# Kernel tuning notes

Hardware: AMD Instinct MI355X
Metric: run time of the kernel (lower is better)

## Reference

```python
import jax, jax.numpy as jnp
import numpy as np

LN_EPS = 1e-5  # torch.nn.LayerNorm default

QLEN, MLEN, BATCH, D_MODEL = 1024, 1024, 8, 1024


def _ft_matrix(qlen, klen):
    """Real part of the causal Fourier matrix (imag part never contributes:
    the input is real and the module takes .real of the product)."""
    ft_len = klen - qlen + 1
    m = jnp.arange(qlen, dtype=jnp.float32)
    k = jnp.arange(ft_len, dtype=jnp.float32)
    base = jnp.cos((2.0 * float(np.pi)) * jnp.outer(m, k) / float(ft_len))
    base = base / float(np.sqrt(ft_len))                      # [qlen, ft_len]
    mat = jnp.pad(base, ((0, 0), (klen - ft_len, 0)))          # left-pad -> [qlen, klen]
    # row i rolled left by (qlen - 1 - i), vectorized as a gather
    shift = (qlen - 1) - jnp.arange(qlen)                      # [qlen]
    cols = (jnp.arange(klen)[None, :] + shift[:, None]) % klen  # [qlen, klen]
    mat = jnp.take_along_axis(mat, cols, axis=1)
    rows = jnp.arange(qlen)[:, None]
    js = jnp.arange(klen)[None, :]
    # tril(diagonal=klen-qlen) AND triu(0)  (same_length=True)
    mask = (js <= rows + (klen - qlen)) & (js >= rows)
    return jnp.where(mask, mat, jnp.float32(0.0))


def setup_inputs() -> dict:
    key = jax.random.key(0)
    k1, k2, k3 = jax.random.split(key, 3)
    return {
        "dec_inp": jax.random.normal(k1, (QLEN, BATCH, D_MODEL), dtype=jnp.float32),
        "pos_emb": jax.random.normal(k2, (QLEN + MLEN, 1, D_MODEL), dtype=jnp.float32),
        "mems": jax.random.normal(k3, (MLEN, BATCH, D_MODEL), dtype=jnp.float32),
        "gamma": jnp.ones((D_MODEL,), dtype=jnp.float32),
        "beta": jnp.zeros((D_MODEL,), dtype=jnp.float32),
        "add_position": 1,
    }


def reference(dec_inp, pos_emb, mems, gamma, beta, add_position):
    qlen = dec_inp.shape[0]
    klen = qlen + mems.shape[0]
    cat = jnp.concatenate([mems, dec_inp], axis=0)  # [klen, b, d]
    if add_position:
        cat = cat + pos_emb  # dropout is identity in eval mode
    ft_mat = _ft_matrix(qlen, klen)                 # [qlen, klen]
    ft = jnp.einsum('ml,lbd->mbd', ft_mat, cat)     # real part of complex matmul
    x = dec_inp + ft / float(np.sqrt(klen))
    mu = jnp.mean(x, axis=-1, keepdims=True)
    var = jnp.var(x, axis=-1, keepdims=True)
    return gamma * (x - mu) * jax.lax.rsqrt(var + LN_EPS) + beta
```

## Files before the change

### kernel.cpp

```cpp
#include <hip/hip_runtime.h>
#include <hip/hip_bf16.h>

#define QLEN   1024
#define MLEN   1024
#define KLEN   2048
#define BATCH  8
#define DMODEL 1024
#define NCOLS  (BATCH * DMODEL)
#define FTLEN  1025

#define BM 128
#define BN 256
#define BK 64
#define NT 18

typedef __attribute__((ext_vector_type(4))) float f32x4;
typedef __attribute__((ext_vector_type(8))) short bf16x8;

typedef __attribute__((address_space(1))) const unsigned int as1_u32;
typedef __attribute__((address_space(3))) unsigned int as3_u32;

static __device__ __forceinline__ unsigned short f2bf(float f) {
    unsigned int u = __builtin_bit_cast(unsigned int, f);
    return (unsigned short)((u + 0x7fffu + ((u >> 16) & 1u)) >> 16);
}
static __device__ __forceinline__ float bf2f(unsigned short s) {
    return __builtin_bit_cast(float, (unsigned int)s << 16);
}
static __device__ __forceinline__ unsigned int packbf(float lo, float hi) {
    return (unsigned int)f2bf(lo) | ((unsigned int)f2bf(hi) << 16);
}

__global__ __launch_bounds__(256) void prep_fused(
    const float* __restrict__ dec, const float* __restrict__ pos,
    const float* __restrict__ mems, const int* __restrict__ addp,
    unsigned short* __restrict__ catT, unsigned short* __restrict__ W)
{
    const int tid = threadIdx.x;
    if (blockIdx.z == 8) {
        const int bchunk = (blockIdx.y * 32 + blockIdx.x) * 4;
#pragma unroll
        for (int r = 0; r < 4; ++r) {
            const int idx = (bchunk + r) * 256 + tid;
            const int m = idx >> 9;
            const int k4 = (idx & 511) * 4;
            union { unsigned short s[4]; int2 v; } u;
#pragma unroll
            for (int j = 0; j < 4; ++j) {
                const int k = k4 + j;
                const int t = k - m;
                float w = 0.0f;
                if (t >= 0 && t < FTLEN) {
                    const int rr = (m * t) % FTLEN;
                    const float x = (float)rr * (1.0f / (float)FTLEN);
                    float c;
                    asm("v_cos_f32 %0, %1" : "=v"(c) : "v"(x));
                    w = c * 0.03123475237772121f;
                }
                u.s[j] = f2bf(w);
            }
            *reinterpret_cast<int2*>(&W[(size_t)m * KLEN + k4]) = u.v;
        }
        return;
    }

    __shared__ unsigned int T2[32 * 68];
    const int lt = blockIdx.x, dt = blockIdx.y, b = blockIdx.z;
    const int l0 = lt * 64, d0 = dt * 64;
    const int add_position = addp[0];

    const int dloc  = (tid & 15) * 4;
    const int lhalf = tid >> 4;

    float4 vc[2][2];
#pragma unroll
    for (int p = 0; p < 2; ++p)
#pragma unroll
        for (int jl = 0; jl < 2; ++jl) {
            const int l = l0 + p * 32 + lhalf * 2 + jl;
            const float* src = (l < MLEN)
                ? (mems + (size_t)l * NCOLS + b * DMODEL + d0 + dloc)
                : (dec + (size_t)(l - MLEN) * NCOLS + b * DMODEL + d0 + dloc);
            vc[p][jl] = *reinterpret_cast<const float4*>(src);
        }
    if (add_position) {
#pragma unroll
        for (int p = 0; p < 2; ++p)
#pragma unroll
            for (int jl = 0; jl < 2; ++jl) {
                const int l = l0 + p * 32 + lhalf * 2 + jl;
                float4 pv = *reinterpret_cast<const float4*>(
                    pos + (size_t)l * DMODEL + d0 + dloc);
                vc[p][jl].x += pv.x; vc[p][jl].y += pv.y;
                vc[p][jl].z += pv.z; vc[p][jl].w += pv.w;
            }
    }
#pragma unroll
    for (int p = 0; p < 2; ++p) {
        const int lp = p * 16 + lhalf;
        uint4 w;
        w.x = packbf(vc[p][0].x, vc[p][1].x);
        w.y = packbf(vc[p][0].y, vc[p][1].y);
        w.z = packbf(vc[p][0].z, vc[p][1].z);
        w.w = packbf(vc[p][0].w, vc[p][1].w);
        *reinterpret_cast<uint4*>(&T2[lp * 68 + dloc]) = w;
    }
    __syncthreads();
    const int d = tid >> 2;
    const size_t n = (size_t)b * DMODEL + d0 + d;
#pragma unroll
    for (int q = 0; q < 2; ++q) {
        const int c8 = (tid & 3) + 4 * q;
        uint4 o;
        o.x = T2[(c8 * 4 + 0) * 68 + d];
        o.y = T2[(c8 * 4 + 1) * 68 + d];
        o.z = T2[(c8 * 4 + 2) * 68 + d];
        o.w = T2[(c8 * 4 + 3) * 68 + d];
        *reinterpret_cast<uint4*>(&catT[n * KLEN + l0 + c8 * 8]) = o;
    }
}

__global__ __launch_bounds__(512) void gemm_band10(
    const unsigned short* __restrict__ W,
    const unsigned short* __restrict__ catT,
    const float* __restrict__ dec,
    unsigned short* __restrict__ xout)
{
    __shared__ unsigned short Alds[3][BM * BK];
    __shared__ unsigned short Blds[3][BN * BK];

    const int tid = threadIdx.x;
    const int wave = tid >> 6, lane = tid & 63;

    const int bid = blockIdx.x;
    const int xcd = bid & 7;
    const int kk = bid >> 3;
    const int m_idx = kk >> 2;
    const int n_idx = xcd * 4 + (kk & 3);
    const int m0 = m_idx * BM, n0 = n_idx * BN;
    const int wm = wave >> 2, wn = wave & 3;

    f32x4 acc[4][4];
    for (int i = 0; i < 4; ++i)
        for (int j = 0; j < 4; ++j)
            acc[i][j] = (f32x4){0.f, 0.f, 0.f, 0.f};

    const int srow = tid >> 3;
    const int scol = (((tid & 7) ^ ((tid >> 3) & 7)) * 8);
    const int fr = lane & 15;
    const int kg = lane >> 4;
    const int rswz = (fr & 7) * 8;

#define STAGE_LOAD_A(S, T, P) do {                                              \
    const int k0_ = m0 + (T) * BK;                                              \
    const int row = (P) * 64 + srow;                                            \
    __builtin_amdgcn_global_load_lds(                                           \
        (as1_u32*)(const void*)(W + (size_t)(m0 + row) * KLEN + k0_ + scol),    \
        (as3_u32*)(void*)(&Alds[S][row * BK + scol]), 16, 0, 0);                \
} while (0)
#define STAGE_LOAD_B(S, T, P) do {                                              \
    const int k0_ = m0 + (T) * BK;                                              \
    const int row = (P) * 64 + srow;                                            \
    __builtin_amdgcn_global_load_lds(                                           \
        (as1_u32*)(const void*)(catT + (size_t)(n0 + row) * KLEN + k0_ + scol), \
        (as3_u32*)(void*)(&Blds[S][row * BK + scol]), 16, 0, 0);                \
} while (0)
#define STAGE_ALL(S, T) do {                                                    \
    STAGE_LOAD_A(S, T, 0); STAGE_LOAD_A(S, T, 1);                               \
    STAGE_LOAD_B(S, T, 0); STAGE_LOAD_B(S, T, 1);                               \
    STAGE_LOAD_B(S, T, 2); STAGE_LOAD_B(S, T, 3);                               \
} while (0)

    STAGE_ALL(0, 0);
    STAGE_ALL(1, 1);

    for (int t = 0; t < NT; ++t) {
        if (t == NT - 1)
            asm volatile("s_waitcnt vmcnt(0)" ::: "memory");
        else
            asm volatile("s_waitcnt vmcnt(6)" ::: "memory");
        __builtin_amdgcn_s_barrier();

        const unsigned short* Ab = Alds[t % 3];
        const unsigned short* Bb = Blds[t % 3];
        const int s2 = (t + 2) % 3;
        const bool pf = (t + 2 < NT);

        {
            bf16x8 a[4], b[4];
#pragma unroll
            for (int f = 0; f < 4; ++f)
                a[f] = *reinterpret_cast<const bf16x8*>(
                    Ab + (wm * 64 + f * 16 + fr) * BK + ((kg * 8) ^ rswz));
#pragma unroll
            for (int f = 0; f < 4; ++f)
                b[f] = *reinterpret_cast<const bf16x8*>(
                    Bb + (wn * 64 + f * 16 + fr) * BK + ((kg * 8) ^ rswz));
            if (pf) { STAGE_LOAD_A(s2, t + 2, 0); STAGE_LOAD_B(s2, t + 2, 0); STAGE_LOAD_B(s2, t + 2, 1); }
            __builtin_amdgcn_s_setprio(1);
#pragma unroll
            for (int fm = 0; fm < 4; ++fm)
#pragma unroll
                for (int fn = 0; fn < 4; ++fn)
                    acc[fm][fn] = __builtin_amdgcn_mfma_f32_16x16x32_bf16(
                        a[fm], b[fn], acc[fm][fn], 0, 0, 0);
            __builtin_amdgcn_s_setprio(0);
        }
        {
            bf16x8 a[4], b[4];
#pragma unroll
            for (int f = 0; f < 4; ++f)
                a[f] = *reinterpret_cast<const bf16x8*>(
                    Ab + (wm * 64 + f * 16 + fr) * BK + ((32 + kg * 8) ^ rswz));
#pragma unroll
            for (int f = 0; f < 4; ++f)
                b[f] = *reinterpret_cast<const bf16x8*>(
                    Bb + (wn * 64 + f * 16 + fr) * BK + ((32 + kg * 8) ^ rswz));
            if (pf) { STAGE_LOAD_A(s2, t + 2, 1); STAGE_LOAD_B(s2, t + 2, 2); STAGE_LOAD_B(s2, t + 2, 3); }
            __builtin_amdgcn_s_setprio(1);
#pragma unroll
            for (int fm = 0; fm < 4; ++fm)
#pragma unroll
                for (int fn = 0; fn < 4; ++fn)
                    acc[fm][fn] = __builtin_amdgcn_mfma_f32_16x16x32_bf16(
                        a[fm], b[fn], acc[fm][fn], 0, 0, 0);
            __builtin_amdgcn_s_setprio(0);
        }
    }
#undef STAGE_ALL
#undef STAGE_LOAD_A
#undef STAGE_LOAD_B

    const float inv = 0.022097086912079612f;
    const int col16 = lane & 15, rquad = lane >> 4;
#pragma unroll
    for (int fm = 0; fm < 4; ++fm)
#pragma unroll
        for (int fn = 0; fn < 4; ++fn)
#pragma unroll
            for (int j = 0; j < 4; ++j) {
                const int m = m0 + wm * 64 + fm * 16 + rquad * 4 + j;
                const int n = n0 + wn * 64 + fn * 16 + col16;
                const size_t o = (size_t)m * NCOLS + n;
                xout[o] = f2bf(dec[o] + acc[fm][fn][j] * inv);
            }
}

__global__ __launch_bounds__(256) void layernorm_rows(
    const unsigned short* __restrict__ x,
    const float* __restrict__ gamma, const float* __restrict__ beta,
    float* __restrict__ out)
{
    __shared__ float ps[4], pq[4];
    const int row = blockIdx.x;
    const int tid = threadIdx.x;
    const size_t base = (size_t)row * DMODEL + tid * 4;
    ushort4 u = *reinterpret_cast<const ushort4*>(x + base);
    float vx = bf2f(u.x), vy = bf2f(u.y), vz = bf2f(u.z), vw = bf2f(u.w);
    float s  = vx + vy + vz + vw;
    float sq = vx * vx + vy * vy + vz * vz + vw * vw;
    for (int off = 32; off > 0; off >>= 1) {
        s  += __shfl_down(s, off);
        sq += __shfl_down(sq, off);
    }
    const int wave = tid >> 6, lane = tid & 63;
    if (lane == 0) { ps[wave] = s; pq[wave] = sq; }
    __syncthreads();
    if (tid == 0) {
        float ts = ps[0] + ps[1] + ps[2] + ps[3];
        float tq = pq[0] + pq[1] + pq[2] + pq[3];
        float mu = ts * (1.0f / DMODEL);
        float var = tq * (1.0f / DMODEL) - mu * mu;
        ps[0] = mu;
        pq[0] = rsqrtf(var + 1e-5f);
    }
    __syncthreads();
    const float mu = ps[0], rs = pq[0];
    float4 g  = *reinterpret_cast<const float4*>(gamma + tid * 4);
    float4 be = *reinterpret_cast<const float4*>(beta + tid * 4);
    float4 o;
    o.x = g.x * (vx - mu) * rs + be.x;
    o.y = g.y * (vy - mu) * rs + be.y;
    o.z = g.z * (vz - mu) * rs + be.z;
    o.w = g.w * (vw - mu) * rs + be.w;
    *reinterpret_cast<float4*>(out + base) = o;
}

extern "C" void kernel_launch(void* const* d_in, const int* in_sizes, int n_in,
                              void* d_out, int out_size, void* d_ws, size_t ws_size,
                              hipStream_t stream)
{
    const float* dec   = (const float*)d_in[0];
    const float* pos   = (const float*)d_in[1];
    const float* mems  = (const float*)d_in[2];
    const float* gamma = (const float*)d_in[3];
    const float* beta  = (const float*)d_in[4];
    const int*   addp  = (const int*)d_in[5];
    float* out = (float*)d_out;

    unsigned short* catT = (unsigned short*)d_ws;
    unsigned short* Wmat = catT + (size_t)NCOLS * KLEN;
    unsigned short* x    = Wmat + (size_t)QLEN * KLEN;

    prep_fused<<<dim3(32, 16, 9), 256, 0, stream>>>(dec, pos, mems, addp, catT, Wmat);
    gemm_band10<<<256, 512, 0, stream>>>(Wmat, catT, dec, x);
    layernorm_rows<<<8192, 256, 0, stream>>>(x, gamma, beta, out);
}
```

Baseline: 60.48 us.

## Reshape banded GEMM tile to 256x128 with 4 waves of 128x64 each

The GEMM block tile changes from 128x256 with 8 waves to 256x128 with 4 waves, and each wave now computes a 128x64 sub-tile with 32 accumulators. The K-band per block grows to 20 steps because the band width follows BM. The aim is more MFMA work per LDS fragment load and fewer waves to synchronise. The cost is extra K work across the wider band, heavier register pressure, and lower occupancy.

```diff
diff --git a/kernel.cpp b/kernel.cpp
--- a/kernel.cpp
+++ b/kernel.cpp
@@ -9,10 +9,10 @@
 #define NCOLS  (BATCH * DMODEL)
 #define FTLEN  1025
 
-#define BM 128
-#define BN 256
+#define BM 256
+#define BN 128
 #define BK 64
-#define NT 18
+#define NT 20
 
 typedef __attribute__((ext_vector_type(4))) float f32x4;
 typedef __attribute__((ext_vector_type(8))) short bf16x8;
@@ -120,7 +120,7 @@
     }
 }
 
-__global__ __launch_bounds__(512) void gemm_band10(
+__global__ __launch_bounds__(256, 1) void gemm_band11(
     const unsigned short* __restrict__ W,
     const unsigned short* __restrict__ catT,
     const float* __restrict__ dec,
@@ -135,13 +135,15 @@
     const int bid = blockIdx.x;
     const int xcd = bid & 7;
     const int kk = bid >> 3;
-    const int m_idx = kk >> 2;
-    const int n_idx = xcd * 4 + (kk & 3);
+    const int m_idx = kk >> 3;
+    const int n_idx = xcd * 8 + (kk & 7);
     const int m0 = m_idx * BM, n0 = n_idx * BN;
-    const int wm = wave >> 2, wn = wave & 3;
-
-    f32x4 acc[4][4];
-    for (int i = 0; i < 4; ++i)
+    const int wm = wave >> 1, wn = wave & 1;
+
+    f32x4 acc[8][4];
+#pragma unroll
+    for (int i = 0; i < 8; ++i)
+#pragma unroll
         for (int j = 0; j < 4; ++j)
             acc[i][j] = (f32x4){0.f, 0.f, 0.f, 0.f};
 
@@ -151,24 +153,24 @@
     const int kg = lane >> 4;
     const int rswz = (fr & 7) * 8;
 
-#define STAGE_LOAD_A(S, T, P) do {                                              \
+#define STAGE_A(S, T, P) do {                                                   \
     const int k0_ = m0 + (T) * BK;                                              \
-    const int row = (P) * 64 + srow;                                            \
+    const int row = (P) * 32 + srow;                                            \
     __builtin_amdgcn_global_load_lds(                                           \
         (as1_u32*)(const void*)(W + (size_t)(m0 + row) * KLEN + k0_ + scol),    \
         (as3_u32*)(void*)(&Alds[S][row * BK + scol]), 16, 0, 0);                \
 } while (0)
-#define STAGE_LOAD_B(S, T, P) do {                                              \
+#define STAGE_B(S, T, P) do {                                                   \
     const int k0_ = m0 + (T) * BK;                                              \
-    const int row = (P) * 64 + srow;                                            \
+    const int row = (P) * 32 + srow;                                            \
     __builtin_amdgcn_global_load_lds(                                           \
         (as1_u32*)(const void*)(catT + (size_t)(n0 + row) * KLEN + k0_ + scol), \
         (as3_u32*)(void*)(&Blds[S][row * BK + scol]), 16, 0, 0);                \
 } while (0)
 #define STAGE_ALL(S, T) do {                                                    \
-    STAGE_LOAD_A(S, T, 0); STAGE_LOAD_A(S, T, 1);                               \
-    STAGE_LOAD_B(S, T, 0); STAGE_LOAD_B(S, T, 1);                               \
-    STAGE_LOAD_B(S, T, 2); STAGE_LOAD_B(S, T, 3);                               \
+    STAGE_A(S, T, 0); STAGE_A(S, T, 1); STAGE_A(S, T, 2); STAGE_A(S, T, 3);     \
+    STAGE_A(S, T, 4); STAGE_A(S, T, 5); STAGE_A(S, T, 6); STAGE_A(S, T, 7);     \
+    STAGE_B(S, T, 0); STAGE_B(S, T, 1); STAGE_B(S, T, 2); STAGE_B(S, T, 3);     \
 } while (0)
 
     STAGE_ALL(0, 0);
@@ -178,7 +180,7 @@
         if (t == NT - 1)
             asm volatile("s_waitcnt vmcnt(0)" ::: "memory");
         else
-            asm volatile("s_waitcnt vmcnt(6)" ::: "memory");
+            asm volatile("s_waitcnt vmcnt(12)" ::: "memory");
         __builtin_amdgcn_s_barrier();
 
         const unsigned short* Ab = Alds[t % 3];
@@ -187,19 +189,23 @@
         const bool pf = (t + 2 < NT);
 
         {
-            bf16x8 a[4], b[4];
-#pragma unroll
-            for (int f = 0; f < 4; ++f)
+            bf16x8 a[8], b[4];
+#pragma unroll
+            for (int f = 0; f < 8; ++f)
                 a[f] = *reinterpret_cast<const bf16x8*>(
-                    Ab + (wm * 64 + f * 16 + fr) * BK + ((kg * 8) ^ rswz));
+                    Ab + (wm * 128 + f * 16 + fr) * BK + ((kg * 8) ^ rswz));
 #pragma unroll
             for (int f = 0; f < 4; ++f)
                 b[f] = *reinterpret_cast<const bf16x8*>(
                     Bb + (wn * 64 + f * 16 + fr) * BK + ((kg * 8) ^ rswz));
-            if (pf) { STAGE_LOAD_A(s2, t + 2, 0); STAGE_LOAD_B(s2, t + 2, 0); STAGE_LOAD_B(s2, t + 2, 1); }
+            if (pf) {
+                STAGE_A(s2, t + 2, 0); STAGE_A(s2, t + 2, 1);
+                STAGE_A(s2, t + 2, 2); STAGE_A(s2, t + 2, 3);
+                STAGE_B(s2, t + 2, 0); STAGE_B(s2, t + 2, 1);
+            }
             __builtin_amdgcn_s_setprio(1);
 #pragma unroll
-            for (int fm = 0; fm < 4; ++fm)
+            for (int fm = 0; fm < 8; ++fm)
 #pragma unroll
                 for (int fn = 0; fn < 4; ++fn)
                     acc[fm][fn] = __builtin_amdgcn_mfma_f32_16x16x32_bf16(
@@ -207,19 +213,23 @@
             __builtin_amdgcn_s_setprio(0);
         }
         {
-            bf16x8 a[4], b[4];
-#pragma unroll
-            for (int f = 0; f < 4; ++f)
+            bf16x8 a[8], b[4];
+#pragma unroll
+            for (int f = 0; f < 8; ++f)
                 a[f] = *reinterpret_cast<const bf16x8*>(
-                    Ab + (wm * 64 + f * 16 + fr) * BK + ((32 + kg * 8) ^ rswz));
+                    Ab + (wm * 128 + f * 16 + fr) * BK + ((32 + kg * 8) ^ rswz));
 #pragma unroll
             for (int f = 0; f < 4; ++f)
                 b[f] = *reinterpret_cast<const bf16x8*>(
                     Bb + (wn * 64 + f * 16 + fr) * BK + ((32 + kg * 8) ^ rswz));
-            if (pf) { STAGE_LOAD_A(s2, t + 2, 1); STAGE_LOAD_B(s2, t + 2, 2); STAGE_LOAD_B(s2, t + 2, 3); }
+            if (pf) {
+                STAGE_A(s2, t + 2, 4); STAGE_A(s2, t + 2, 5);
+                STAGE_A(s2, t + 2, 6); STAGE_A(s2, t + 2, 7);
+                STAGE_B(s2, t + 2, 2); STAGE_B(s2, t + 2, 3);
+            }
             __builtin_amdgcn_s_setprio(1);
 #pragma unroll
-            for (int fm = 0; fm < 4; ++fm)
+            for (int fm = 0; fm < 8; ++fm)
 #pragma unroll
                 for (int fn = 0; fn < 4; ++fn)
                     acc[fm][fn] = __builtin_amdgcn_mfma_f32_16x16x32_bf16(
@@ -228,18 +238,18 @@
         }
     }
 #undef STAGE_ALL
-#undef STAGE_LOAD_A
-#undef STAGE_LOAD_B
+#undef STAGE_A
+#undef STAGE_B
 
     const float inv = 0.022097086912079612f;
     const int col16 = lane & 15, rquad = lane >> 4;
 #pragma unroll
-    for (int fm = 0; fm < 4; ++fm)
+    for (int fm = 0; fm < 8; ++fm)
 #pragma unroll
         for (int fn = 0; fn < 4; ++fn)
 #pragma unroll
             for (int j = 0; j < 4; ++j) {
-                const int m = m0 + wm * 64 + fm * 16 + rquad * 4 + j;
+                const int m = m0 + wm * 128 + fm * 16 + rquad * 4 + j;
                 const int n = n0 + wn * 64 + fn * 16 + col16;
                 const size_t o = (size_t)m * NCOLS + n;
                 xout[o] = f2bf(dec[o] + acc[fm][fn][j] * inv);
@@ -303,6 +313,6 @@
     unsigned short* x    = Wmat + (size_t)QLEN * KLEN;
 
     prep_fused<<<dim3(32, 16, 9), 256, 0, stream>>>(dec, pos, mems, addp, catT, Wmat);
-    gemm_band10<<<256, 512, 0, stream>>>(Wmat, catT, dec, x);
+    gemm_band11<<<256, 256, 0, stream>>>(Wmat, catT, dec, x);
     layernorm_rows<<<8192, 256, 0, stream>>>(x, gamma, beta, out);
 }
```

New measurement: 66.93 us. +10.7%, slower.
